# Kernel optimization log

Measured on AMD Instinct MI355X. Metric: run time of the kernel, lower is better.

## Reference

```python
import jax, jax.numpy as jnp
import numpy as np

H = 8            # kv heads
R = 2            # qhead_ratio -> hq = 16 query heads
D = 128          # head_size
DEG = 2          # power degree
GATE_OFFSET = 6.906768  # ~log(999), gates start near 1


def setup_inputs() -> dict:
    key = jax.random.key(0)
    ks = jax.random.split(key, 7)
    B, T, C = 1, 2048, 2048
    q_dim = H * R * D   # 2048
    kv_dim = H * D      # 1024
    s = 0.02
    return {
        "hidden_states": jax.random.normal(ks[0], (B, T, C), dtype=jnp.float32),
        "Wq": jax.random.normal(ks[1], (C, q_dim), dtype=jnp.float32) * s,
        "Wk": jax.random.normal(ks[2], (C, kv_dim), dtype=jnp.float32) * s,
        "Wv": jax.random.normal(ks[3], (C, kv_dim), dtype=jnp.float32) * s,
        "Wg": jax.random.normal(ks[4], (C, H), dtype=jnp.float32) * s,
        "Wc": jax.random.normal(ks[5], (q_dim, C), dtype=jnp.float32) * s,
        "bc": jnp.zeros((C,), dtype=jnp.float32),
    }


def _power_attention(q, k, v, log_g):
    # q: [B,T,hq,D], k/v: [B,T,H,D], log_g: [B,T,H]
    B, T, hq, d = q.shape
    scale = 1.0 / d ** 0.5
    # GQA: query head i uses kv head i // R (q was viewed as (B,T,H,R,D))
    k = jnp.repeat(k, R, axis=2)            # [B,T,hq,D]
    v = jnp.repeat(v, R, axis=2)            # [B,T,hq,D]
    logG = jnp.cumsum(log_g, axis=1)        # [B,T,H]
    logG = jnp.repeat(logG, R, axis=2)      # [B,T,hq]
    logG = jnp.transpose(logG, (0, 2, 1))   # [B,hq,T]
    qk = jnp.einsum('bthd,bshd->bhts', q, k) * scale   # [B,hq,T,T]
    a = qk ** DEG                                       # even degree -> >= 0
    # gating decay exp(logG_t - logG_s) <= 1 for s <= t
    gate = logG[:, :, :, None] - logG[:, :, None, :]    # [B,hq,T,T]
    causal = jnp.tril(jnp.ones((T, T), dtype=bool))
    a = jnp.where(causal, a * jnp.exp(gate), 0.0)
    norm = jnp.sum(a, axis=-1) + 1e-6                   # [B,hq,T]
    y = jnp.einsum('bhts,bshd->bthd', a, v)             # [B,T,hq,D]
    y = y / jnp.transpose(norm, (0, 2, 1))[..., None]
    return y


def reference(hidden_states, Wq, Wk, Wv, Wg, Wc, bc):
    B, T, C = hidden_states.shape
    q = (hidden_states @ Wq).reshape(B, T, H * R, D)
    k = (hidden_states @ Wk).reshape(B, T, H, D)
    v = (hidden_states @ Wv).reshape(B, T, H, D)
    g = hidden_states @ Wg                              # [B,T,H]
    log_g = jax.nn.log_sigmoid(GATE_OFFSET + g.astype(jnp.float32))
    y = _power_attention(q, k, v, log_g)                # [B,T,hq,D]
    y = y.reshape(B, T, H * R * D)
    return y @ Wc + bc
```

## Files before the change

### kernel.cpp

```cpp
#include <hip/hip_runtime.h>

typedef unsigned short u16;
typedef unsigned int u32;
typedef unsigned long long u64;
typedef __bf16 bf16x8 __attribute__((ext_vector_type(8)));
typedef float f32x4 __attribute__((ext_vector_type(4)));

union FragAB {
  bf16x8 v;
  u16 u[8];
  u32 w[4];
  u64 d2[2];
};

__device__ __forceinline__ u16 f2bf(float f) {
  u32 u = __builtin_bit_cast(u32, f);
  u += 0x7fffu + ((u >> 16) & 1u);
  return (u16)(u >> 16);
}

__device__ __forceinline__ void gload_lds16(const void* g, void* l) {
  __builtin_amdgcn_global_load_lds((__attribute__((address_space(1))) void*)g,
                                   (__attribute__((address_space(3))) void*)l, 16, 0, 0);
}

__device__ __forceinline__ int permcol(int n) {
  int k = n & 31;
  return (n & ~31) | ((k & 12) << 1) | ((k & 16) >> 2) | (k & 3);
}

__global__ __launch_bounds__(256) void fused_conv_gate(const float* __restrict__ hs,
                                                       const float* __restrict__ Wg,
                                                       u16* __restrict__ out,
                                                       float* __restrict__ lgt) {
  int lane = threadIdx.x & 63, wid = threadIdx.x >> 6;
  int t = blockIdx.x * 4 + wid;
  const float* row = hs + (size_t)t * 2048;
  u16* orow = out + (size_t)t * 2048;
  float acc[8] = {0.f, 0.f, 0.f, 0.f, 0.f, 0.f, 0.f, 0.f};
#pragma unroll
  for (int j = 0; j < 8; j++) {
    int c = j * 256 + lane * 4;
    float4 v = *(const float4*)&row[c];
    u64 pk = (u64)f2bf(v.x) | ((u64)f2bf(v.y) << 16) | ((u64)f2bf(v.z) << 32) |
             ((u64)f2bf(v.w) << 48);
    int g = (c >> 2) & 7;
    int ncol = (c & ~31) | ((2 * (g & 3) + (g >> 2)) << 2);
    *(u64*)&orow[ncol] = pk;
#pragma unroll
    for (int e = 0; e < 4; e++) {
      float x = (e == 0) ? v.x : (e == 1) ? v.y : (e == 2) ? v.z : v.w;
      float4 w0 = *(const float4*)&Wg[(c + e) * 8];
      float4 w1 = *(const float4*)&Wg[(c + e) * 8 + 4];
      acc[0] += x * w0.x; acc[1] += x * w0.y; acc[2] += x * w0.z; acc[3] += x * w0.w;
      acc[4] += x * w1.x; acc[5] += x * w1.y; acc[6] += x * w1.z; acc[7] += x * w1.w;
    }
  }
#pragma unroll
  for (int h = 0; h < 8; h++) {
    float v = acc[h];
    for (int m = 1; m < 64; m <<= 1) v += __shfl_xor(v, m, 64);
    if (lane == 0) {
      float x = 6.906768f + v;
      lgt[h * 2048 + t] = -log1pf(__expf(-x));
    }
  }
}

__global__ __launch_bounds__(256) void tconv_kernel(const float* __restrict__ in,
                                                    u16* __restrict__ out, int K, int N) {
  __shared__ float tile[64][65];
  int col = threadIdx.x & 63;
  int r0 = threadIdx.x >> 6;
  int kb = blockIdx.y * 64, nb = blockIdx.x * 64;
  int pcol = permcol(col);
#pragma unroll
  for (int i = 0; i < 16; i++) {
    int r = r0 + i * 4;
    tile[r][col] = in[(size_t)(kb + r) * N + nb + col];
  }
  __syncthreads();
#pragma unroll
  for (int i = 0; i < 16; i++) {
    int r = r0 + i * 4;
    out[(size_t)(nb + r) * K + kb + pcol] = f2bf(tile[col][r]);
  }
}

__global__ __launch_bounds__(256) void tconv3_kernel(const float* __restrict__ Wq,
                                                     const float* __restrict__ Wk,
                                                     const float* __restrict__ Wv,
                                                     u16* __restrict__ slab) {
  const int z = blockIdx.z;
  if (z > 0 && blockIdx.x >= 16) return;
  __shared__ float tile[64][65];
  const float* src = (z == 0) ? Wq : (z == 1 ? Wk : Wv);
  const int srcN = (z == 0) ? 2048 : 1024;
  const int dstRowBase = (z == 0) ? 0 : (z == 1 ? 2048 : 3072);
  int col = threadIdx.x & 63;
  int r0 = threadIdx.x >> 6;
  int kb = blockIdx.y * 64, nb = blockIdx.x * 64;
  int pcol = permcol(col);
#pragma unroll
  for (int i = 0; i < 16; i++) {
    int r = r0 + i * 4;
    tile[r][col] = src[(size_t)(kb + r) * srcN + nb + col];
  }
  __syncthreads();
#pragma unroll
  for (int i = 0; i < 16; i++) {
    int r = r0 + i * 4;
    slab[(size_t)(dstRowBase + nb + r) * 2048 + kb + pcol] = f2bf(tile[col][r]);
  }
}

__global__ __launch_bounds__(256) void cumsum_kernel(const float* __restrict__ lgt,
                                                     float* __restrict__ scTab) {
  int h = blockIdx.x;
  __shared__ float buf[2048];
  for (int i = threadIdx.x; i < 2048; i += 256) buf[i] = lgt[h * 2048 + i];
  __syncthreads();
  for (int off = 1; off < 2048; off <<= 1) {
    float tmp[8];
#pragma unroll
    for (int j = 0; j < 8; j++) {
      int i = threadIdx.x + j * 256;
      tmp[j] = (i >= off) ? buf[i - off] : 0.f;
    }
    __syncthreads();
#pragma unroll
    for (int j = 0; j < 8; j++) {
      int i = threadIdx.x + j * 256;
      buf[i] += tmp[j];
    }
    __syncthreads();
  }
  for (int i = threadIdx.x; i < 2048; i += 256) {
    float lg = buf[i];
    scTab[i * 16 + h] = __expf(0.5f * lg) * 0.08838834764831845f;
    scTab[i * 16 + 8 + h] = __expf(-0.5f * lg);
  }
}

template <int MODE, int NT>
__global__ __launch_bounds__(512, 4) void gemm_v4(const u16* __restrict__ A,
                                                  const u16* __restrict__ BT,
                                                  void* __restrict__ C0,
                                                  void* __restrict__ C1,
                                                  const float* __restrict__ scTab,
                                                  int permLim) {
  __shared__ __align__(16) u16 As[2 * 128 * 64];
  __shared__ __align__(16) u16 Bs[2 * 128 * 64];
  constexpr int nwg = 16 * NT * (MODE == 2 ? 2 : 1);
  constexpr int cpx = nwg >> 3;
  const int raw = (int)blockIdx.x;
  const int wg = (raw & 7) * cpx + (raw >> 3);
  int bx, by, z;
  if constexpr (MODE == 2) {
    z = wg & 1;
    int t = wg >> 1;
    by = t >> 4;
    bx = t & 15;
  } else {
    z = 0;
    by = wg >> 4;
    bx = wg & 15;
  }
  const int kBeg = (MODE == 2) ? z * 1024 : 0;
  const int kEnd = (MODE == 2) ? kBeg + 1024 : 2048;
  constexpr int N = NT * 128;

  const int tid = threadIdx.x;
  const int lane = tid & 63, wid = tid >> 6;
  const int m0 = bx * 128, n0 = by * 128;
  const int wr = wid >> 2, wc = wid & 3;
  const int l15 = lane & 15, kg = lane >> 4;

  f32x4 acc[4][2];
#pragma unroll
  for (int i = 0; i < 4; i++)
#pragma unroll
    for (int j = 0; j < 2; j++) acc[i][j] = f32x4{0.f, 0.f, 0.f, 0.f};

  const int c0 = (wid * 2) * 64 + lane;
  const int c1 = c0 + 64;
  const int r0 = c0 >> 3, s0u = (c0 & 7) ^ (r0 & 7);
  const int r1 = c1 >> 3, s1u = (c1 & 7) ^ (r1 & 7);
  const u16* Asrc0 = A + (size_t)(m0 + r0) * 2048 + s0u * 8;
  const u16* Asrc1 = A + (size_t)(m0 + r1) * 2048 + s1u * 8;
  const u16* Bsrc0 = BT + (size_t)(n0 + r0) * 2048 + s0u * 8;
  const u16* Bsrc1 = BT + (size_t)(n0 + r1) * 2048 + s1u * 8;

  auto stage = [&](int buf, int k0) {
    u16* Ad = As + buf * 8192 + (wid * 2) * 512;
    u16* Bd = Bs + buf * 8192 + (wid * 2) * 512;
    gload_lds16(Asrc0 + k0, Ad);
    gload_lds16(Asrc1 + k0, Ad + 512);
    gload_lds16(Bsrc0 + k0, Bd);
    gload_lds16(Bsrc1 + k0, Bd + 512);
  };

  stage(0, kBeg);

  int cur = 0;
  for (int k0 = kBeg; k0 < kEnd; k0 += 64) {
    const bool hasNext = (k0 + 64 < kEnd);
    if (hasNext) {
      stage(cur ^ 1, k0 + 64);
      asm volatile("s_waitcnt vmcnt(4)" ::: "memory");
    } else {
      asm volatile("s_waitcnt vmcnt(0)" ::: "memory");
    }
    __builtin_amdgcn_sched_barrier(0);
    __builtin_amdgcn_s_barrier();
    __builtin_amdgcn_sched_barrier(0);

    const u16* Ab = As + cur * 8192;
    const u16* Bb = Bs + cur * 8192;
#pragma unroll
    for (int ks = 0; ks < 2; ks++) {
      FragAB af[4], bfr[2];
#pragma unroll
      for (int mt = 0; mt < 4; mt++) {
        int row = wr * 64 + mt * 16 + l15;
        af[mt].v = *(const bf16x8*)&Ab[row * 64 + 8 * ((ks * 4 + kg) ^ (row & 7))];
      }
#pragma unroll
      for (int nt = 0; nt < 2; nt++) {
        int row = wc * 32 + nt * 16 + l15;
        bfr[nt].v = *(const bf16x8*)&Bb[row * 64 + 8 * ((ks * 4 + kg) ^ (row & 7))];
      }
#pragma unroll
      for (int mt = 0; mt < 4; mt++)
#pragma unroll
        for (int nt = 0; nt < 2; nt++)
          acc[mt][nt] = __builtin_amdgcn_mfma_f32_16x16x32_bf16(af[mt].v, bfr[nt].v, acc[mt][nt], 0, 0, 0);
    }
    __builtin_amdgcn_sched_barrier(0);
    __builtin_amdgcn_s_barrier();
    cur ^= 1;
  }

#pragma unroll
  for (int mt = 0; mt < 4; mt++) {
#pragma unroll
    for (int re = 0; re < 4; re++) {
      int m = m0 + wr * 64 + mt * 16 + kg * 4 + re;
#pragma unroll
      for (int nt = 0; nt < 2; nt++) {
        int n = n0 + wc * 32 + nt * 16 + l15;
        float v = acc[mt][nt][re];
        if constexpr (MODE == 2) {
          u16* P = z ? (u16*)C1 : (u16*)C0;
          P[(size_t)m * N + n] = f2bf(v);
        } else {
          int code = (n < 2048) ? (n >> 8) : ((n < 3072) ? (8 + ((n - 2048) >> 7)) : -1);
          if (code >= 0) v *= scTab[(size_t)m * 16 + code];
          int nw = (n < permLim) ? permcol(n) : n;
          ((u16*)C0)[(size_t)m * N + nw] = f2bf(v);
        }
      }
    }
  }
}

__global__ __launch_bounds__(256, 2) void power_attn(const u16* __restrict__ QKV,
                                                     u16* __restrict__ y0b,
                                                     u16* __restrict__ y1b,
                                                     float* __restrict__ npart) {
  __shared__ __align__(16) u16 Ks[2 * 64 * 128];
  __shared__ __align__(16) u16 Vt[2 * 128 * 64];

  const int raw = (int)blockIdx.x;
  const int x = raw & 7;
  const int k = raw >> 3;
  const int hq = x * 2 + (k >> 5);
  const int kk = k & 31;
  const int half = kk & 1;
  const int bslot = kk >> 1;
  const int qa = (bslot + x * 3) & 15;
  const int qt = half ? (15 - qa) : qa;
  const int hk = hq >> 1;
  const int t0 = qt * 128;

  const int tid = threadIdx.x, lane = tid & 63, wid = tid >> 6;
  const int l15 = lane & 15, kg = lane >> 4;
  const int l7 = l15 & 7;

  const int s4 = tid & 15, dgrp = tid >> 4;
  const int ubase = 4 * (s4 >> 3) + (s4 & 3);
  const int vhb = (s4 >> 2) & 1;

  const u16* Kbase = QKV + 2048 + hk * 128;
  const u16* Vbase = QKV + 3072 + hk * 128 + dgrp * 8;

  FragAB qf[2][4];
  int myT[2];
#pragma unroll
  for (int cg = 0; cg < 2; cg++) {
    myT[cg] = t0 + wid * 16 + cg * 64 + l15;
    const u16* qrow = QKV + (size_t)myT[cg] * 4096 + hq * 128;
#pragma unroll
    for (int ks = 0; ks < 4; ks++) qf[cg][ks].v = *(const bf16x8*)(qrow + ks * 32 + kg * 8);
  }

  FragAB ones;
#pragma unroll
  for (int i = 0; i < 8; i++) ones.u[i] = 0x3F80u;

  f32x4 yacc[8][2];
#pragma unroll
  for (int i = 0; i < 8; i++)
#pragma unroll
    for (int c = 0; c < 2; c++) yacc[i][c] = f32x4{0.f, 0.f, 0.f, 0.f};
  f32x4 nrm[2] = {f32x4{0.f, 0.f, 0.f, 0.f}, f32x4{0.f, 0.f, 0.f, 0.f}};

  const int itBeg = half ? (qt + 1) : 0;
  const int itEnd = half ? (2 * qt + 2) : (qt + 1);

  auto stageK = [&](int s0, int bb) {
#pragma unroll
    for (int c = 0; c < 4; c++) {
      int ch = (wid * 4 + c) * 64 + lane;
      int row = ch >> 4, du = ch & 15;
      int su = du ^ (row & 7);
      gload_lds16(Kbase + (size_t)(s0 + row) * 4096 + su * 8, &Ks[bb * 8192 + (wid * 4 + c) * 512]);
    }
  };
  auto loadV = [&](int s0, uint4* vr) {
#pragma unroll
    for (int r = 0; r < 4; r++) vr[r] = *(const uint4*)(Vbase + (size_t)(s0 + 4 * s4 + r) * 4096);
  };
  auto writeV = [&](int bb, const uint4* vr) {
    u16* vd = &Vt[bb * 8192];
    const u32* w0 = (const u32*)&vr[0];
    const u32* w1 = (const u32*)&vr[1];
    const u32* w2 = (const u32*)&vr[2];
    const u32* w3 = (const u32*)&vr[3];
#pragma unroll
    for (int i = 0; i < 8; i++) {
      u32 sel = (i & 1) ? 0x07060302u : 0x05040100u;
      u32 lo = __builtin_amdgcn_perm(w1[i >> 1], w0[i >> 1], sel);
      u32 hi = __builtin_amdgcn_perm(w3[i >> 1], w2[i >> 1], sel);
      int d = dgrp * 8 + i;
      int e = d * 64 + 8 * (ubase ^ i) + 4 * vhb;
      *(u64*)&vd[e] = (u64)lo | ((u64)hi << 32);
    }
  };

  {
    uint4 vr[4];
    stageK(itBeg * 64, 0);
    loadV(itBeg * 64, vr);
    writeV(0, vr);
  }
  __syncthreads();

  for (int it = itBeg; it < itEnd; it++) {
    const int cur = (it - itBeg) & 1;
    const int s0 = it * 64;
    const bool hasNext = (it + 1 < itEnd);
    uint4 vr[4];
    if (hasNext) {
      stageK(s0 + 64, cur ^ 1);
      loadV(s0 + 64, vr);
    }

    const u16* kb = &Ks[cur * 8192];
    f32x4 sacc[4][2];
#pragma unroll
    for (int mt = 0; mt < 4; mt++)
#pragma unroll
      for (int cg = 0; cg < 2; cg++) sacc[mt][cg] = f32x4{0.f, 0.f, 0.f, 0.f};
    __builtin_amdgcn_s_setprio(1);
#pragma unroll
    for (int ks = 0; ks < 4; ks++) {
#pragma unroll
      for (int mt = 0; mt < 4; mt++) {
        FragAB af;
        af.v = *(const bf16x8*)&kb[(mt * 16 + l15) * 128 + 8 * ((4 * ks + kg) ^ l7)];
        sacc[mt][0] = __builtin_amdgcn_mfma_f32_16x16x32_bf16(af.v, qf[0][ks].v, sacc[mt][0], 0, 0, 0);
        sacc[mt][1] = __builtin_amdgcn_mfma_f32_16x16x32_bf16(af.v, qf[1][ks].v, sacc[mt][1], 0, 0, 0);
      }
    }
    __builtin_amdgcn_s_setprio(0);

    FragAB pa[2][2];
    const bool need_mask = (it >= 2 * qt);
#pragma unroll
    for (int mt = 0; mt < 4; mt++) {
#pragma unroll
      for (int cg = 0; cg < 2; cg++) {
        u32 pb[4];
#pragma unroll
        for (int r = 0; r < 4; r++) {
          float x2 = sacc[mt][cg][r];
          float p = x2 * x2;
          if (need_mask) {
            int s = s0 + mt * 16 + kg * 4 + r;
            p = (s <= myT[cg]) ? p : 0.f;
          }
          pb[r] = __builtin_bit_cast(u32, p) + 0x8000u;
        }
        pa[cg][mt >> 1].w[(mt & 1) * 2 + 0] = __builtin_amdgcn_perm(pb[1], pb[0], 0x07060302u);
        pa[cg][mt >> 1].w[(mt & 1) * 2 + 1] = __builtin_amdgcn_perm(pb[3], pb[2], 0x07060302u);
      }
    }

    const u16* vb = &Vt[cur * 8192];
    const int x0 = 8 * (kg ^ l7);
    __builtin_amdgcn_s_setprio(1);
#pragma unroll
    for (int ksv = 0; ksv < 2; ksv++) {
      const int xo = x0 ^ (ksv * 32);
#pragma unroll
      for (int nt = 0; nt < 8; nt++) {
        FragAB bfv;
        bfv.v = *(const bf16x8*)&vb[(nt * 16 + l15) * 64 + xo];
        yacc[nt][0] = __builtin_amdgcn_mfma_f32_16x16x32_bf16(pa[0][ksv].v, bfv.v, yacc[nt][0], 0, 0, 0);
        yacc[nt][1] = __builtin_amdgcn_mfma_f32_16x16x32_bf16(pa[1][ksv].v, bfv.v, yacc[nt][1], 0, 0, 0);
      }
      nrm[0] = __builtin_amdgcn_mfma_f32_16x16x32_bf16(pa[0][ksv].v, ones.v, nrm[0], 0, 0, 0);
      nrm[1] = __builtin_amdgcn_mfma_f32_16x16x32_bf16(pa[1][ksv].v, ones.v, nrm[1], 0, 0, 0);
    }
    __builtin_amdgcn_s_setprio(0);

    if (hasNext) writeV(cur ^ 1, vr);
    __syncthreads();
  }

  u16* yb = half ? y1b : y0b;
  float* np = npart + half * (16 * 2048);
#pragma unroll
  for (int cg = 0; cg < 2; cg++) {
    if (l15 == 0) {
#pragma unroll
      for (int re = 0; re < 4; re++)
        np[hq * 2048 + t0 + wid * 16 + cg * 64 + kg * 4 + re] = nrm[cg][re];
    }
#pragma unroll
    for (int re = 0; re < 4; re++) {
      int trow = t0 + wid * 16 + cg * 64 + kg * 4 + re;
      u16* yrow = yb + (size_t)trow * 2048 + hq * 128;
#pragma unroll
      for (int nt = 0; nt < 8; nt++) yrow[nt * 16 + l15] = f2bf(yacc[nt][cg][re]);
    }
  }
}

__global__ __launch_bounds__(256) void combine_kernel(const u16* __restrict__ y0b,
                                                      const u16* __restrict__ y1b,
                                                      const float* __restrict__ npart,
                                                      u16* __restrict__ yb) {
  int i = blockIdx.x * 256 + threadIdx.x;
  int e0 = i << 2;
  int t = e0 >> 11;
  int hq = (e0 >> 7) & 15;
  int nidx = hq * 2048 + t;
  float nn = npart[nidx] + npart[32768 + nidx] + 1e-6f;
  float inv = 1.0f / nn;
  u64 a0 = *(const u64*)&y0b[e0];
  u64 a1 = *(const u64*)&y1b[e0];
  float r[4];
#pragma unroll
  for (int j = 0; j < 4; j++) {
    float v0 = __builtin_bit_cast(float, (u32)((a0 >> (16 * j)) & 0xffffu) << 16);
    float v1 = __builtin_bit_cast(float, (u32)((a1 >> (16 * j)) & 0xffffu) << 16);
    r[j] = (v0 + v1) * inv;
  }
  u64 pk = (u64)f2bf(r[0]) | ((u64)f2bf(r[1]) << 16) | ((u64)f2bf(r[2]) << 32) |
           ((u64)f2bf(r[3]) << 48);
  int col = e0 & 2047;
  int g = (col >> 2) & 7;
  int ncol = (col & ~31) | ((2 * (g & 3) + (g >> 2)) << 2);
  *(u64*)&yb[(size_t)t * 2048 + ncol] = pk;
}

__global__ __launch_bounds__(256) void combine2_kernel(const u16* __restrict__ p0,
                                                       const u16* __restrict__ p1,
                                                       float* __restrict__ out,
                                                       const float* __restrict__ bias) {
  int i = blockIdx.x * 256 + threadIdx.x;
  int e0 = i << 2;
  int col = e0 & 2047;
  u64 a0 = *(const u64*)&p0[e0];
  u64 a1 = *(const u64*)&p1[e0];
  float4 bb = *(const float4*)&bias[col];
  float4 r;
#pragma unroll
  for (int j = 0; j < 4; j++) {
    float v0 = __builtin_bit_cast(float, (u32)((a0 >> (16 * j)) & 0xffffu) << 16);
    float v1 = __builtin_bit_cast(float, (u32)((a1 >> (16 * j)) & 0xffffu) << 16);
    float bj = (j == 0) ? bb.x : (j == 1) ? bb.y : (j == 2) ? bb.z : bb.w;
    ((float*)&r)[j] = v0 + v1 + bj;
  }
  ((float4*)out)[i] = r;
}

extern "C" void kernel_launch(void* const* d_in, const int* in_sizes, int n_in,
                              void* d_out, int out_size, void* d_ws, size_t ws_size,
                              hipStream_t stream) {
  (void)in_sizes; (void)n_in; (void)out_size; (void)ws_size;
  const float* hs = (const float*)d_in[0];
  const float* Wq = (const float*)d_in[1];
  const float* Wk = (const float*)d_in[2];
  const float* Wv = (const float*)d_in[3];
  const float* Wg = (const float*)d_in[4];
  const float* Wc = (const float*)d_in[5];
  const float* bc = (const float*)d_in[6];
  float* out = (float*)d_out;

  char* ws = (char*)d_ws;
  const size_t MB = 1024 * 1024;
  u16* slab   = (u16*)(ws);
  u16* hs_bf  = (u16*)(ws + 16 * MB);
  u16* y_bf   = (u16*)(ws + 16 * MB);
  u16* qkv_bf = (u16*)(ws + 24 * MB);
  u16* p0h    = (u16*)(ws + 24 * MB);
  u16* p1h    = (u16*)(ws + 32 * MB);
  u16* y0b    = (u16*)(ws + 40 * MB);
  float* lgt   = (float*)(ws + 56 * MB);
  float* scTab = (float*)(ws + 56 * MB + 65536);
  float* npart = (float*)(ws + 56 * MB + 65536 + 131072);
  u16* y1b = (u16*)out;
  u16* WcT = slab;

  fused_conv_gate<<<512, 256, 0, stream>>>(hs, Wg, hs_bf, lgt);
  cumsum_kernel<<<8, 256, 0, stream>>>(lgt, scTab);
  tconv3_kernel<<<dim3(32, 32, 3), 256, 0, stream>>>(Wq, Wk, Wv, slab);

  gemm_v4<1, 32><<<512, 512, 0, stream>>>(hs_bf, slab, qkv_bf, nullptr, scTab, 3072);

  tconv_kernel<<<dim3(32, 32), 256, 0, stream>>>(Wc, WcT, 2048, 2048);

  power_attn<<<dim3(512), 256, 0, stream>>>(qkv_bf, y0b, y1b, npart);
  combine_kernel<<<4096, 256, 0, stream>>>(y0b, y1b, npart, y_bf);

  gemm_v4<2, 16><<<512, 512, 0, stream>>>(y_bf, WcT, p0h, p1h, nullptr, 0);
  combine2_kernel<<<4096, 256, 0, stream>>>(p0h, p1h, out, bc);
}
```

Baseline: 165.5 us.

## Widen GEMM tiles to 128x256 with triple-buffered K=32 LDS pipeline

Result: slower. 181.9 us (+9.9%).

```diff
diff --git a/kernel.cpp b/kernel.cpp
--- a/kernel.cpp
+++ b/kernel.cpp
@@ -28,6 +28,8 @@
   int k = n & 31;
   return (n & ~31) | ((k & 12) << 1) | ((k & 16) >> 2) | (k & 3);
 }
+
+__device__ __forceinline__ int swz32(int r) { return (r & 3) ^ ((r >> 2) & 3); }
 
 __global__ __launch_bounds__(256) void fused_conv_gate(const float* __restrict__ hs,
                                                        const float* __restrict__ Wg,
@@ -142,16 +144,16 @@
   }
 }
 
-template <int MODE, int NT>
-__global__ __launch_bounds__(512, 4) void gemm_v4(const u16* __restrict__ A,
+template <int MODE, int NOUT>
+__global__ __launch_bounds__(512, 2) void gemm_v6(const u16* __restrict__ A,
                                                   const u16* __restrict__ BT,
                                                   void* __restrict__ C0,
                                                   void* __restrict__ C1,
                                                   const float* __restrict__ scTab,
                                                   int permLim) {
-  __shared__ __align__(16) u16 As[2 * 128 * 64];
-  __shared__ __align__(16) u16 Bs[2 * 128 * 64];
-  constexpr int nwg = 16 * NT * (MODE == 2 ? 2 : 1);
+  __shared__ __align__(16) u16 As[3 * 128 * 32];
+  __shared__ __align__(16) u16 Bs[3 * 256 * 32];
+  constexpr int nwg = 256;
   constexpr int cpx = nwg >> 3;
   const int raw = (int)blockIdx.x;
   const int wg = (raw & 7) * cpx + (raw >> 3);
@@ -159,55 +161,89 @@
   if constexpr (MODE == 2) {
     z = wg & 1;
     int t = wg >> 1;
+    bx = t & 15;
     by = t >> 4;
-    bx = t & 15;
   } else {
     z = 0;
+    bx = wg & 15;
     by = wg >> 4;
-    bx = wg & 15;
   }
   const int kBeg = (MODE == 2) ? z * 1024 : 0;
-  const int kEnd = (MODE == 2) ? kBeg + 1024 : 2048;
-  constexpr int N = NT * 128;
+  constexpr int T = (MODE == 2) ? 32 : 64;
 
   const int tid = threadIdx.x;
   const int lane = tid & 63, wid = tid >> 6;
-  const int m0 = bx * 128, n0 = by * 128;
+  const int m0 = bx * 128, n0 = by * 256;
   const int wr = wid >> 2, wc = wid & 3;
   const int l15 = lane & 15, kg = lane >> 4;
 
-  f32x4 acc[4][2];
+  f32x4 acc[4][4];
 #pragma unroll
   for (int i = 0; i < 4; i++)
 #pragma unroll
-    for (int j = 0; j < 2; j++) acc[i][j] = f32x4{0.f, 0.f, 0.f, 0.f};
-
-  const int c0 = (wid * 2) * 64 + lane;
-  const int c1 = c0 + 64;
-  const int r0 = c0 >> 3, s0u = (c0 & 7) ^ (r0 & 7);
-  const int r1 = c1 >> 3, s1u = (c1 & 7) ^ (r1 & 7);
-  const u16* Asrc0 = A + (size_t)(m0 + r0) * 2048 + s0u * 8;
-  const u16* Asrc1 = A + (size_t)(m0 + r1) * 2048 + s1u * 8;
-  const u16* Bsrc0 = BT + (size_t)(n0 + r0) * 2048 + s0u * 8;
-  const u16* Bsrc1 = BT + (size_t)(n0 + r1) * 2048 + s1u * 8;
-
-  auto stage = [&](int buf, int k0) {
-    u16* Ad = As + buf * 8192 + (wid * 2) * 512;
-    u16* Bd = Bs + buf * 8192 + (wid * 2) * 512;
-    gload_lds16(Asrc0 + k0, Ad);
-    gload_lds16(Asrc1 + k0, Ad + 512);
-    gload_lds16(Bsrc0 + k0, Bd);
-    gload_lds16(Bsrc1 + k0, Bd + 512);
+    for (int j = 0; j < 4; j++) acc[i][j] = f32x4{0.f, 0.f, 0.f, 0.f};
+
+  const int chA = wid * 64 + lane;
+  const int rA = chA >> 2, duA = chA & 3;
+  const u16* srcA = A + (size_t)(m0 + rA) * 2048 + kBeg + (duA ^ swz32(rA)) * 8;
+  u16* dstA = As + wid * 512;
+  const u16* srcB0;
+  const u16* srcB1;
+  u16* dstB0;
+  u16* dstB1;
+  {
+    int ch0 = (wid * 2) * 64 + lane;
+    int r0_ = ch0 >> 2, du0 = ch0 & 3;
+    srcB0 = BT + (size_t)(n0 + r0_) * 2048 + kBeg + (du0 ^ swz32(r0_)) * 8;
+    dstB0 = Bs + (wid * 2) * 512;
+    int ch1 = ch0 + 64;
+    int r1_ = ch1 >> 2, du1 = ch1 & 3;
+    srcB1 = BT + (size_t)(n0 + r1_) * 2048 + kBeg + (du1 ^ swz32(r1_)) * 8;
+    dstB1 = Bs + (wid * 2 + 1) * 512;
+  }
+
+  auto stage = [&](int buf, int kt) {
+    gload_lds16(srcA + kt * 32, dstA + buf * 4096);
+    gload_lds16(srcB0 + kt * 32, dstB0 + buf * 8192);
+    gload_lds16(srcB1 + kt * 32, dstB1 + buf * 8192);
   };
 
-  stage(0, kBeg);
+  int offA[4], offB[4];
+#pragma unroll
+  for (int mt = 0; mt < 4; mt++) {
+    int row = wr * 64 + mt * 16 + l15;
+    offA[mt] = row * 32 + (kg ^ swz32(row)) * 8;
+  }
+#pragma unroll
+  for (int nt = 0; nt < 4; nt++) {
+    int row = wc * 64 + nt * 16 + l15;
+    offB[nt] = row * 32 + (kg ^ swz32(row)) * 8;
+  }
+
+  stage(0, 0);
+  stage(1, 1);
+  asm volatile("s_waitcnt vmcnt(3)" ::: "memory");
+  __builtin_amdgcn_sched_barrier(0);
+  __builtin_amdgcn_s_barrier();
+  __builtin_amdgcn_sched_barrier(0);
 
   int cur = 0;
-  for (int k0 = kBeg; k0 < kEnd; k0 += 64) {
-    const bool hasNext = (k0 + 64 < kEnd);
-    if (hasNext) {
-      stage(cur ^ 1, k0 + 64);
-      asm volatile("s_waitcnt vmcnt(4)" ::: "memory");
+  for (int t = 0; t < T; t++) {
+    const u16* Ab = As + cur * 4096;
+    const u16* Bb = Bs + cur * 8192;
+    FragAB af[4], bfr[4];
+#pragma unroll
+    for (int mt = 0; mt < 4; mt++) af[mt].v = *(const bf16x8*)&Ab[offA[mt]];
+#pragma unroll
+    for (int nt = 0; nt < 4; nt++) bfr[nt].v = *(const bf16x8*)&Bb[offB[nt]];
+
+    if (t + 2 < T) {
+      int nxt = cur + 2;
+      if (nxt >= 3) nxt -= 3;
+      stage(nxt, t + 2);
+    }
+    if (t < T - 2) {
+      asm volatile("s_waitcnt vmcnt(3)" ::: "memory");
     } else {
       asm volatile("s_waitcnt vmcnt(0)" ::: "memory");
     }
@@ -215,30 +251,17 @@
     __builtin_amdgcn_s_barrier();
     __builtin_amdgcn_sched_barrier(0);
 
-    const u16* Ab = As + cur * 8192;
-    const u16* Bb = Bs + cur * 8192;
-#pragma unroll
-    for (int ks = 0; ks < 2; ks++) {
-      FragAB af[4], bfr[2];
-#pragma unroll
-      for (int mt = 0; mt < 4; mt++) {
-        int row = wr * 64 + mt * 16 + l15;
-        af[mt].v = *(const bf16x8*)&Ab[row * 64 + 8 * ((ks * 4 + kg) ^ (row & 7))];
-      }
-#pragma unroll
-      for (int nt = 0; nt < 2; nt++) {
-        int row = wc * 32 + nt * 16 + l15;
-        bfr[nt].v = *(const bf16x8*)&Bb[row * 64 + 8 * ((ks * 4 + kg) ^ (row & 7))];
-      }
-#pragma unroll
-      for (int mt = 0; mt < 4; mt++)
-#pragma unroll
-        for (int nt = 0; nt < 2; nt++)
-          acc[mt][nt] = __builtin_amdgcn_mfma_f32_16x16x32_bf16(af[mt].v, bfr[nt].v, acc[mt][nt], 0, 0, 0);
-    }
+    __builtin_amdgcn_s_setprio(1);
+#pragma unroll
+    for (int mt = 0; mt < 4; mt++)
+#pragma unroll
+      for (int nt = 0; nt < 4; nt++)
+        acc[mt][nt] = __builtin_amdgcn_mfma_f32_16x16x32_bf16(af[mt].v, bfr[nt].v, acc[mt][nt], 0, 0, 0);
+    __builtin_amdgcn_s_setprio(0);
     __builtin_amdgcn_sched_barrier(0);
     __builtin_amdgcn_s_barrier();
-    cur ^= 1;
+    __builtin_amdgcn_sched_barrier(0);
+    cur = (cur == 2) ? 0 : cur + 1;
   }
 
 #pragma unroll
@@ -247,17 +270,17 @@
     for (int re = 0; re < 4; re++) {
       int m = m0 + wr * 64 + mt * 16 + kg * 4 + re;
 #pragma unroll
-      for (int nt = 0; nt < 2; nt++) {
-        int n = n0 + wc * 32 + nt * 16 + l15;
+      for (int nt = 0; nt < 4; nt++) {
+        int n = n0 + wc * 64 + nt * 16 + l15;
         float v = acc[mt][nt][re];
         if constexpr (MODE == 2) {
           u16* P = z ? (u16*)C1 : (u16*)C0;
-          P[(size_t)m * N + n] = f2bf(v);
+          P[(size_t)m * NOUT + n] = f2bf(v);
         } else {
           int code = (n < 2048) ? (n >> 8) : ((n < 3072) ? (8 + ((n - 2048) >> 7)) : -1);
           if (code >= 0) v *= scTab[(size_t)m * 16 + code];
           int nw = (n < permLim) ? permcol(n) : n;
-          ((u16*)C0)[(size_t)m * N + nw] = f2bf(v);
+          ((u16*)C0)[(size_t)m * NOUT + nw] = f2bf(v);
         }
       }
     }
@@ -529,13 +552,13 @@
   cumsum_kernel<<<8, 256, 0, stream>>>(lgt, scTab);
   tconv3_kernel<<<dim3(32, 32, 3), 256, 0, stream>>>(Wq, Wk, Wv, slab);
 
-  gemm_v4<1, 32><<<512, 512, 0, stream>>>(hs_bf, slab, qkv_bf, nullptr, scTab, 3072);
+  gemm_v6<1, 4096><<<256, 512, 0, stream>>>(hs_bf, slab, qkv_bf, nullptr, scTab, 3072);
 
   tconv_kernel<<<dim3(32, 32), 256, 0, stream>>>(Wc, WcT, 2048, 2048);
 
   power_attn<<<dim3(512), 256, 0, stream>>>(qkv_bf, y0b, y1b, npart);
   combine_kernel<<<4096, 256, 0, stream>>>(y0b, y1b, npart, y_bf);
 
-  gemm_v4<2, 16><<<512, 512, 0, stream>>>(y_bf, WcT, p0h, p1h, nullptr, 0);
+  gemm_v6<2, 2048><<<256, 512, 0, stream>>>(y_bf, WcT, p0h, p1h, nullptr, 0);
   combine2_kernel<<<4096, 256, 0, stream>>>(p0h, p1h, out, bc);
 }
```

## Load GEMM B fragments directly from global into registers, halve LDS

Applied to the files above, without the earlier changes.

New measurement: 218.2 us. 31.8% more time.

```diff
diff --git a/kernel.cpp b/kernel.cpp
--- a/kernel.cpp
+++ b/kernel.cpp
@@ -143,14 +143,13 @@
 }
 
 template <int MODE, int NT>
-__global__ __launch_bounds__(512, 4) void gemm_v4(const u16* __restrict__ A,
+__global__ __launch_bounds__(512, 4) void gemm_v8(const u16* __restrict__ A,
                                                   const u16* __restrict__ BT,
                                                   void* __restrict__ C0,
                                                   void* __restrict__ C1,
                                                   const float* __restrict__ scTab,
                                                   int permLim) {
   __shared__ __align__(16) u16 As[2 * 128 * 64];
-  __shared__ __align__(16) u16 Bs[2 * 128 * 64];
   constexpr int nwg = 16 * NT * (MODE == 2 ? 2 : 1);
   constexpr int cpx = nwg >> 3;
   const int raw = (int)blockIdx.x;
@@ -167,7 +166,7 @@
     bx = wg & 15;
   }
   const int kBeg = (MODE == 2) ? z * 1024 : 0;
-  const int kEnd = (MODE == 2) ? kBeg + 1024 : 2048;
+  constexpr int KT = (MODE == 2) ? 16 : 32;
   constexpr int N = NT * 128;
 
   const int tid = threadIdx.x;
@@ -188,58 +187,80 @@
   const int r1 = c1 >> 3, s1u = (c1 & 7) ^ (r1 & 7);
   const u16* Asrc0 = A + (size_t)(m0 + r0) * 2048 + s0u * 8;
   const u16* Asrc1 = A + (size_t)(m0 + r1) * 2048 + s1u * 8;
-  const u16* Bsrc0 = BT + (size_t)(n0 + r0) * 2048 + s0u * 8;
-  const u16* Bsrc1 = BT + (size_t)(n0 + r1) * 2048 + s1u * 8;
-
-  auto stage = [&](int buf, int k0) {
+
+  auto stageA = [&](int buf, int k0) {
     u16* Ad = As + buf * 8192 + (wid * 2) * 512;
-    u16* Bd = Bs + buf * 8192 + (wid * 2) * 512;
     gload_lds16(Asrc0 + k0, Ad);
     gload_lds16(Asrc1 + k0, Ad + 512);
-    gload_lds16(Bsrc0 + k0, Bd);
-    gload_lds16(Bsrc1 + k0, Bd + 512);
   };
 
-  stage(0, kBeg);
-
-  int cur = 0;
-  for (int k0 = kBeg; k0 < kEnd; k0 += 64) {
-    const bool hasNext = (k0 + 64 < kEnd);
-    if (hasNext) {
-      stage(cur ^ 1, k0 + 64);
-      asm volatile("s_waitcnt vmcnt(4)" ::: "memory");
-    } else {
-      asm volatile("s_waitcnt vmcnt(0)" ::: "memory");
-    }
-    __builtin_amdgcn_sched_barrier(0);
-    __builtin_amdgcn_s_barrier();
-    __builtin_amdgcn_sched_barrier(0);
-
-    const u16* Ab = As + cur * 8192;
-    const u16* Bb = Bs + cur * 8192;
+  const u16* Brow0 = BT + (size_t)(n0 + wc * 32 + l15) * 2048 + kg * 8;
+  const u16* Brow1 = BT + (size_t)(n0 + wc * 32 + 16 + l15) * 2048 + kg * 8;
+
+  FragAB bA[4], bB[4];
+#define LOADB(b, k0)                                   \
+  do {                                                 \
+    (b)[0].v = *(const bf16x8*)(Brow0 + (k0));         \
+    (b)[1].v = *(const bf16x8*)(Brow0 + (k0) + 32);    \
+    (b)[2].v = *(const bf16x8*)(Brow1 + (k0));         \
+    (b)[3].v = *(const bf16x8*)(Brow1 + (k0) + 32);    \
+  } while (0)
+
+  auto compute = [&](int buf, FragAB (&b)[4]) {
+    const u16* Ab = As + buf * 8192;
 #pragma unroll
     for (int ks = 0; ks < 2; ks++) {
-      FragAB af[4], bfr[2];
+      FragAB af[4];
 #pragma unroll
       for (int mt = 0; mt < 4; mt++) {
         int row = wr * 64 + mt * 16 + l15;
         af[mt].v = *(const bf16x8*)&Ab[row * 64 + 8 * ((ks * 4 + kg) ^ (row & 7))];
       }
 #pragma unroll
-      for (int nt = 0; nt < 2; nt++) {
-        int row = wc * 32 + nt * 16 + l15;
-        bfr[nt].v = *(const bf16x8*)&Bb[row * 64 + 8 * ((ks * 4 + kg) ^ (row & 7))];
-      }
-#pragma unroll
-      for (int mt = 0; mt < 4; mt++)
-#pragma unroll
-        for (int nt = 0; nt < 2; nt++)
-          acc[mt][nt] = __builtin_amdgcn_mfma_f32_16x16x32_bf16(af[mt].v, bfr[nt].v, acc[mt][nt], 0, 0, 0);
-    }
-    __builtin_amdgcn_sched_barrier(0);
-    __builtin_amdgcn_s_barrier();
-    cur ^= 1;
-  }
+      for (int mt = 0; mt < 4; mt++) {
+        acc[mt][0] = __builtin_amdgcn_mfma_f32_16x16x32_bf16(af[mt].v, b[ks].v, acc[mt][0], 0, 0, 0);
+        acc[mt][1] = __builtin_amdgcn_mfma_f32_16x16x32_bf16(af[mt].v, b[2 + ks].v, acc[mt][1], 0, 0, 0);
+      }
+    }
+  };
+
+  stageA(0, kBeg);
+  LOADB(bA, kBeg);
+
+  for (int t = 0; t < KT; t += 2) {
+    {
+      stageA(1, kBeg + (t + 1) * 64);
+      LOADB(bB, kBeg + (t + 1) * 64);
+      asm volatile("s_waitcnt vmcnt(6)" ::: "memory");
+      __builtin_amdgcn_sched_barrier(0);
+      __builtin_amdgcn_s_barrier();
+      __builtin_amdgcn_sched_barrier(0);
+      __builtin_amdgcn_s_setprio(1);
+      compute(0, bA);
+      __builtin_amdgcn_s_setprio(0);
+      __builtin_amdgcn_sched_barrier(0);
+      __builtin_amdgcn_s_barrier();
+    }
+    {
+      const bool hn = (t + 2 < KT);
+      if (hn) {
+        stageA(0, kBeg + (t + 2) * 64);
+        LOADB(bA, kBeg + (t + 2) * 64);
+        asm volatile("s_waitcnt vmcnt(6)" ::: "memory");
+      } else {
+        asm volatile("s_waitcnt vmcnt(0)" ::: "memory");
+      }
+      __builtin_amdgcn_sched_barrier(0);
+      __builtin_amdgcn_s_barrier();
+      __builtin_amdgcn_sched_barrier(0);
+      __builtin_amdgcn_s_setprio(1);
+      compute(1, bB);
+      __builtin_amdgcn_s_setprio(0);
+      __builtin_amdgcn_sched_barrier(0);
+      __builtin_amdgcn_s_barrier();
+    }
+  }
+#undef LOADB
 
 #pragma unroll
   for (int mt = 0; mt < 4; mt++) {
@@ -529,13 +550,13 @@
   cumsum_kernel<<<8, 256, 0, stream>>>(lgt, scTab);
   tconv3_kernel<<<dim3(32, 32, 3), 256, 0, stream>>>(Wq, Wk, Wv, slab);
 
-  gemm_v4<1, 32><<<512, 512, 0, stream>>>(hs_bf, slab, qkv_bf, nullptr, scTab, 3072);
+  gemm_v8<1, 32><<<512, 512, 0, stream>>>(hs_bf, slab, qkv_bf, nullptr, scTab, 3072);
 
   tconv_kernel<<<dim3(32, 32), 256, 0, stream>>>(Wc, WcT, 2048, 2048);
 
   power_attn<<<dim3(512), 256, 0, stream>>>(qkv_bf, y0b, y1b, npart);
   combine_kernel<<<4096, 256, 0, stream>>>(y0b, y1b, npart, y_bf);
 
-  gemm_v4<2, 16><<<512, 512, 0, stream>>>(y_bf, WcT, p0h, p1h, nullptr, 0);
+  gemm_v8<2, 16><<<512, 512, 0, stream>>>(y_bf, WcT, p0h, p1h, nullptr, 0);
   combine2_kernel<<<4096, 256, 0, stream>>>(p0h, p1h, out, bc);
 }
```
